# Performance work log

Measured on AMD Instinct MI355X. Metric: run time of the kernel, lower is better.

Reference implementation:

```python
import jax, jax.numpy as jnp
from jax import lax
import numpy as np

R = 4            # search_range
B, H, W, C = 8, 192, 192, 64
CV = (2 * R + 1) ** 2          # 81 cost-volume channels
CIN0 = CV + 2 * C              # concat(cost, prv, nxt) channels = 209
FILTERS = (128, 64, 32, 16)
DN = ('NHWC', 'HWIO', 'NHWC')
EPS = 1e-3                     # Keras BatchNormalization default epsilon


def setup_inputs() -> dict:
    key = jax.random.key(0)
    ks = iter(jax.random.split(key, 32))
    inp = {}
    inp['prv'] = jax.random.normal(next(ks), (B, H, W, C), jnp.float32)
    inp['nxt'] = jax.random.normal(next(ks), (B, H, W, C), jnp.float32)
    cin = CIN0
    for i, f in enumerate(FILTERS):
        inp[f'dw{i}'] = jax.random.normal(next(ks), (3, 3, 1, cin), jnp.float32) / np.sqrt(9.0)
        inp[f'pw{i}'] = jax.random.normal(next(ks), (1, 1, cin, f), jnp.float32) / np.sqrt(cin)
        inp[f'b{i}'] = jnp.zeros((f,), jnp.float32)
        cin = f
    inp['bn_gamma'] = jnp.ones((cin,), jnp.float32)
    inp['bn_beta'] = jnp.zeros((cin,), jnp.float32)
    inp['bn_mean'] = jnp.zeros((cin,), jnp.float32)
    inp['bn_var'] = jnp.ones((cin,), jnp.float32)
    inp['flow_w'] = jax.random.normal(next(ks), (3, 3, cin, 2), jnp.float32) / np.sqrt(9.0 * cin)
    return inp


def mish(x):
    return x * jnp.tanh(jax.nn.softplus(x))


def cost_volume(prv, nxt):
    # pad nxt by R on spatial dims, correlate over (2R+1)^2 shifts
    pad = jnp.pad(nxt, ((0, 0), (R, R), (R, R), (0, 0)))
    vols = []
    for i in range(2 * R + 1):           # fixed 9x9 offset set (not a data dim)
        for j in range(2 * R + 1):
            roi = lax.slice(pad, (0, i, j, 0), (B, i + H, j + W, C))
            vols.append(jnp.mean(prv * roi, axis=-1))
    cv = jnp.stack(vols, axis=-1)        # [B,H,W,81]
    return jax.nn.leaky_relu(cv, 0.1)


def sep_conv(x, dw, pw, b):
    cin = x.shape[-1]
    y = lax.conv_general_dilated(x, dw, (1, 1), 'SAME',
                                 dimension_numbers=DN, feature_group_count=cin)
    y = lax.conv_general_dilated(y, pw, (1, 1), 'SAME', dimension_numbers=DN) + b
    return mish(y)


def reference(prv, nxt, dw0, pw0, b0, dw1, pw1, b1, dw2, pw2, b2, dw3, pw3, b3,
              bn_gamma, bn_beta, bn_mean, bn_var, flow_w):
    cost = cost_volume(prv, nxt)
    x = jnp.concatenate([cost, prv, nxt], axis=-1)   # [B,H,W,209]
    for dw, pw, b in ((dw0, pw0, b0), (dw1, pw1, b1), (dw2, pw2, b2), (dw3, pw3, b3)):
        x = sep_conv(x, dw, pw, b)
    # BatchNorm (inference: moving statistics)
    x = (x - bn_mean) * (bn_gamma / jnp.sqrt(bn_var + EPS)) + bn_beta
    flow = lax.conv_general_dilated(x, flow_w, (1, 1), 'SAME', dimension_numbers=DN)
    scale = (float(H) ** 2 + float(W) ** 2) ** 0.5
    return scale * flow
```

## Files before the change

kernel.cpp:

```cpp
#include <hip/hip_runtime.h>
#include <hip/hip_bf16.h>

#define BB 8
#define HH 192
#define WW 192
#define CC0 64
#define NPIX (BB*HH*WW)
#define NCV 81
#define CVP 96

typedef __attribute__((ext_vector_type(8))) short short8;
typedef __attribute__((ext_vector_type(4))) short short4v;
typedef __attribute__((ext_vector_type(4))) float f32x4;

__device__ __forceinline__ float bf2f(short s) {
    union { unsigned u; float f; } x; x.u = ((unsigned)(unsigned short)s) << 16; return x.f;
}
__device__ __forceinline__ short f2bf(float f) {
    __hip_bfloat16 h = __float2bfloat16(f);
    return *reinterpret_cast<short*>(&h);
}
__device__ __forceinline__ void cvt8(const short8 iv, float* fv) {
    const int* ip = (const int*)&iv;
#pragma unroll
    for (int e = 0; e < 4; ++e) {
        union { unsigned u; float f; } lo, hi;
        lo.u = ((unsigned)ip[e]) << 16;
        hi.u = ((unsigned)ip[e]) & 0xffff0000u;
        fv[2 * e] = lo.f; fv[2 * e + 1] = hi.f;
    }
}

__device__ __forceinline__ float mish_f(float v) {
    if (v > 20.0f) return v;
    const float u = __expf(v);
    const float n = u * (u + 2.0f);
    return v * n / (n + 2.0f);
}

__global__ __launch_bounds__(256) void prep_kernel(
    const float* __restrict__ dw0, const float* __restrict__ pw0,
    const float* __restrict__ dw1, const float* __restrict__ pw1,
    const float* __restrict__ dw2, const float* __restrict__ pw2,
    const float* __restrict__ dw3, const float* __restrict__ pw3,
    __hip_bfloat16* __restrict__ wout)
{
    const int u = blockIdx.x * 256 + threadIdx.x;
    if (u >= 43456) return;
    float v = 0.f;
    if (u < 2016) {
        const int t = u / 224, c = u % 224;
        if (c < 64)       v = dw0[t*209 + 81  + c];
        else if (c < 128) v = dw0[t*209 + 145 + (c-64)];
        else if (c < 209) v = dw0[t*209 + (c-128)];
    } else if (u < 3168) {
        const int r = u-2016, t = r/128, c = r%128; v = dw1[t*128+c];
    } else if (u < 3744) {
        const int r = u-3168, t = r/64, c = r%64; v = dw2[t*64+c];
    } else if (u < 4032) {
        const int r = u-3744, t = r/32, c = r%32; v = dw3[t*32+c];
    } else if (u < 32704) {
        const int r = u-4032, n = r/224, c = r%224;
        if (c < 64)       v = pw0[(81+c)*128 + n];
        else if (c < 128) v = pw0[(145+(c-64))*128 + n];
        else if (c < 209) v = pw0[(c-128)*128 + n];
    } else if (u < 40896) {
        const int r = u-32704, n = r/128, c = r%128; v = pw1[c*64 + n];
    } else if (u < 42944) {
        const int r = u-40896, n = r/64, c = r%64; v = pw2[c*32 + n];
    } else {
        const int r = u-42944, n = r/32, c = r%32; v = pw3[c*16 + n];
    }
    wout[u] = __float2bfloat16(v);
}

__global__ __launch_bounds__(256) void prep2_kernel(
    const float* __restrict__ dw0, const float* __restrict__ dw1,
    const float* __restrict__ dw2, const float* __restrict__ dw3,
    const float* __restrict__ bn_g, const float* __restrict__ bn_b,
    const float* __restrict__ bn_m, const float* __restrict__ bn_v,
    const float* __restrict__ fw, float* __restrict__ fout)
{
    const int u = blockIdx.x * 256 + threadIdx.x;
    if (u >= 4338) return;
    float v = 0.f;
    if (u < 2016) {
        const int t = u / 224, c = u % 224;
        if (c < 64)       v = dw0[t*209 + 81  + c];
        else if (c < 128) v = dw0[t*209 + 145 + (c-64)];
        else if (c < 209) v = dw0[t*209 + (c-128)];
    } else if (u < 3168) {
        const int r = u-2016, t = r/128, c = r%128; v = dw1[t*128+c];
    } else if (u < 3744) {
        const int r = u-3168, t = r/64, c = r%64; v = dw2[t*64+c];
    } else if (u < 4032) {
        const int r = u-3744, t = r/32, c = r%32; v = dw3[t*32+c];
    } else if (u < 4320) {
        const int r = u-4032, t = r/32, rem = r%32, c = rem >> 1, s = rem & 1;
        const float sc = bn_g[c] * rsqrtf(bn_v[c] + 1e-3f);
        v = sc * fw[t*32 + c*2 + s];
    } else {
        const int r = u-4320, t = r/2, s = r%2;
        float a = 0.f;
        for (int c = 0; c < 16; ++c) {
            const float sc = bn_g[c] * rsqrtf(bn_v[c] + 1e-3f);
            const float sh = bn_b[c] - bn_m[c] * sc;
            a += sh * fw[t*32 + c*2 + s];
        }
        v = a;
    }
    fout[u] = v;
}

template<int UNIFIED>
__global__ __launch_bounds__(256) void cost_mfma_kernel(
    const float* __restrict__ prv, const float* __restrict__ nxt,
    __hip_bfloat16* __restrict__ xout)
{
    constexpr int OST   = UNIFIED ? 224 : CVP;
    constexpr int CVOFF = UNIFIED ? 128 : 0;

    __shared__ __align__(16) short sNxt[2][48][70];
    __shared__ __align__(16) short sCv[4][32][96];

    const int tid  = threadIdx.x;
    const int lane = tid & 63;
    const int wv   = tid >> 6;
    const int ln15 = lane & 15;
    const int kq   = lane >> 4;
    const int mt   = wv & 1;
    const int jt   = wv >> 1;

    const int bx = blockIdx.x;
    const int tw = bx % 6;
    const int th = (bx / 6) % 48;
    const int b  = bx / 288;
    const int w0 = tw * 32, h0 = th * 4;

    {
        const short8 z = {0,0,0,0,0,0,0,0};
#pragma unroll
        for (int t = 0; t < 6; ++t) {
            const int idx = tid + t * 256;
            const int row = idx / 384, rem = idx % 384;
            const int px = rem / 12, c8 = rem % 12;
            *(short8*)&sCv[row][px][c8 * 8] = z;
        }
    }

    short8 af0[4], af1[4];
    {
        const int apx = w0 + mt * 16 + ln15;
#pragma unroll
        for (int r4 = 0; r4 < 4; ++r4) {
            const float* ap = prv + (((size_t)b * HH + h0 + r4) * WW + apx) * CC0 + kq * 8;
            const float4 x0 = *(const float4*)(ap);
            const float4 x1 = *(const float4*)(ap + 4);
            const float4 x2 = *(const float4*)(ap + 32);
            const float4 x3 = *(const float4*)(ap + 36);
            af0[r4][0]=f2bf(x0.x); af0[r4][1]=f2bf(x0.y); af0[r4][2]=f2bf(x0.z); af0[r4][3]=f2bf(x0.w);
            af0[r4][4]=f2bf(x1.x); af0[r4][5]=f2bf(x1.y); af0[r4][6]=f2bf(x1.z); af0[r4][7]=f2bf(x1.w);
            af1[r4][0]=f2bf(x2.x); af1[r4][1]=f2bf(x2.y); af1[r4][2]=f2bf(x2.z); af1[r4][3]=f2bf(x2.w);
            af1[r4][4]=f2bf(x3.x); af1[r4][5]=f2bf(x3.y); af1[r4][6]=f2bf(x3.z); af1[r4][7]=f2bf(x3.w);
        }
    }

    const int s_px = (tid & 0xFF) >> 4;

    int cur = 0;
    {
        const int y0 = h0 - 4;
        if ((unsigned)y0 < (unsigned)HH) {
            const float* rowp = nxt + (((size_t)b * HH + y0) * WW) * CC0;
#pragma unroll
            for (int t = 0; t < 3; ++t) {
                const int u = tid + t * 256;
                if (u < 640) {
                    const int px = u >> 4, c4 = u & 15;
                    const int gw = w0 - 4 + px;
                    float4 v = make_float4(0.f, 0.f, 0.f, 0.f);
                    if ((unsigned)gw < (unsigned)WW)
                        v = *(const float4*)(rowp + (size_t)gw * CC0 + c4 * 4);
                    short4v sv;
                    sv[0]=f2bf(v.x); sv[1]=f2bf(v.y); sv[2]=f2bf(v.z); sv[3]=f2bf(v.w);
                    *(short4v*)&sNxt[0][px][c4 * 4] = sv;
                }
            }
        }
    }

    const size_t obase_blk = (((size_t)b * HH + h0) * WW + w0);

    for (int i = 0; i < 12; ++i) {
        const int y = h0 - 4 + i;
        const bool yok = ((unsigned)y < (unsigned)HH);
        __syncthreads();

        const int yn = y + 1;
        const bool nok = (i < 11) && ((unsigned)yn < (unsigned)HH);
        float4 sreg[3];
        if (nok) {
            const float* rowp = nxt + (((size_t)b * HH + yn) * WW) * CC0;
#pragma unroll
            for (int t = 0; t < 3; ++t) {
                const int u = tid + t * 256;
                sreg[t] = make_float4(0.f, 0.f, 0.f, 0.f);
                if (u < 640) {
                    const int px = u >> 4, c4 = u & 15;
                    const int gw = w0 - 4 + px;
                    if ((unsigned)gw < (unsigned)WW)
                        sreg[t] = *(const float4*)(rowp + (size_t)gw * CC0 + c4 * 4);
                }
            }
        }

        if (yok) {
            const int nb = mt * 16 + jt * 16 + ln15;
            const short* bp = &sNxt[cur][nb][kq * 8];
            const short8 b0 = *(const short8*)bp;
            const short8 b1 = *(const short8*)(bp + 32);
#pragma unroll
            for (int r4 = 0; r4 < 4; ++r4) {
                const int h = h0 + r4;
                const int rband = y - h + 4;
                if ((unsigned)rband <= 8u) {
                    f32x4 acc = {0.f, 0.f, 0.f, 0.f};
                    acc = __builtin_amdgcn_mfma_f32_16x16x32_bf16(af0[r4], b0, acc, 0, 0, 0);
                    acc = __builtin_amdgcn_mfma_f32_16x16x32_bf16(af1[r4], b1, acc, 0, 0, 0);
#pragma unroll
                    for (int rr = 0; rr < 4; ++rr) {
                        const int m_local = kq * 4 + rr;
                        const int dj = jt * 16 + ln15 - m_local;
                        if ((unsigned)dj < 9u) {
                            float mv = acc[rr] * (1.0f / 64.0f);
                            mv = (mv > 0.f) ? mv : 0.1f * mv;
                            sCv[r4][mt * 16 + m_local][rband * 9 + dj] = f2bf(mv);
                        }
                    }
                }
            }
            if (UNIFIED && y >= h0 && y < h0 + 4) {
                const int px_o = tid >> 3, cg = tid & 7;
                short* op = (short*)xout + (((size_t)b * HH + y) * WW + w0 + px_o) * OST
                            + 64 + cg * 8;
                *(short8*)op = *(const short8*)&sNxt[cur][4 + px_o][cg * 8];
            }
        }

        if (nok) {
#pragma unroll
            for (int t = 0; t < 3; ++t) {
                const int u = tid + t * 256;
                if (u < 640) {
                    const int px = u >> 4, c4 = u & 15;
                    short4v sv;
                    sv[0]=f2bf(sreg[t].x); sv[1]=f2bf(sreg[t].y);
                    sv[2]=f2bf(sreg[t].z); sv[3]=f2bf(sreg[t].w);
                    *(short4v*)&sNxt[cur ^ 1][px][c4 * 4] = sv;
                }
            }
        }
        cur ^= 1;
    }

    __syncthreads();
#pragma unroll
    for (int t = 0; t < 6; ++t) {
        const int idx = tid + t * 256;
        const int row = idx / 384, rem = idx % 384;
        const int px = rem / 12, c8 = rem % 12;
        short* op = (short*)xout + (obase_blk + (size_t)row * WW + px) * OST + CVOFF + c8 * 8;
        *(short8*)op = *(const short8*)&sCv[row][px][c8 * 8];
    }
    if (UNIFIED) {
#pragma unroll
        for (int t = 0; t < 4; ++t) {
            const int u = tid + t * 256;
            const int row = u >> 8, px = (u >> 3) & 31, cg = u & 7;
            const float* ap = prv + (obase_blk + (size_t)row * WW + px) * CC0 + cg * 8;
            const float4 x0 = *(const float4*)(ap);
            const float4 x1 = *(const float4*)(ap + 4);
            short8 v;
            v[0]=f2bf(x0.x); v[1]=f2bf(x0.y); v[2]=f2bf(x0.z); v[3]=f2bf(x0.w);
            v[4]=f2bf(x1.x); v[5]=f2bf(x1.y); v[6]=f2bf(x1.z); v[7]=f2bf(x1.w);
            short* op = (short*)xout + (obase_blk + (size_t)row * WW + px) * OST + cg * 8;
            *(short8*)op = v;
        }
    }
}

template<int KP, int COUT, int MODE>
__global__ __launch_bounds__(256) void sepconv_mfma(
    const __hip_bfloat16* __restrict__ in,
    const float* __restrict__ prv, const float* __restrict__ nxt,
    const float* __restrict__ dwf,
    const __hip_bfloat16* __restrict__ Bt,
    const float* __restrict__ bias,
    __hip_bfloat16* __restrict__ out)
{
    constexpr int NT  = COUT / 16;
    constexpr int WGN = (NT >= 2) ? 2 : 1;
    constexpr int WGM = 4 / WGN;
    constexpr int TM  = 8 / WGM;
    constexpr int TN  = NT / WGN;

    __shared__ __align__(16) short sIn[6][34][32];
    __shared__ __align__(16) short sA[4][128][8];
    __shared__ __align__(16) short sB[4][COUT][8];

    const int tid  = threadIdx.x;
    const int lane = tid & 63;
    const int wv   = tid >> 6;
    const int ln15 = lane & 15;
    const int kq   = lane >> 4;
    const int wm   = wv % WGM;
    const int wn   = wv / WGM;

    const int bx = blockIdx.x;
    const int tw = bx % 6;
    const int th = (bx / 6) % 48;
    const int bb = bx / 288;
    const int w0 = tw * 32, h0 = th * 4;

    const int dkbu = __builtin_amdgcn_readfirstlane(wv);
    const int dww  = lane & 31;
    const int dhh  = (lane >> 5) * 2;

    f32x4 acc[TM][TN] = {};

    for (int k0 = 0; k0 < KP; k0 += 32) {
        for (int u = tid; u < 816; u += 256) {
            const int kb = u & 3;
            const int p  = u >> 2;
            const int iw = p % 34, ih = p / 34;
            const int gw = w0 - 1 + iw, gh = h0 - 1 + ih;
            short8 v = {0,0,0,0,0,0,0,0};
            if ((unsigned)gw < (unsigned)WW && (unsigned)gh < (unsigned)HH) {
                const size_t pix = ((size_t)bb * HH + gh) * WW + gw;
                const int c0 = k0 + kb * 8;
                if (MODE == 0) {
                    v = *(const short8*)((const short*)in + pix * KP + c0);
                } else {
                    if (c0 < 64) {
                        const float4* s = (const float4*)(prv + pix * 64 + c0);
                        const float4 a = s[0], bq = s[1];
                        v[0]=f2bf(a.x);  v[1]=f2bf(a.y);  v[2]=f2bf(a.z);  v[3]=f2bf(a.w);
                        v[4]=f2bf(bq.x); v[5]=f2bf(bq.y); v[6]=f2bf(bq.z); v[7]=f2bf(bq.w);
                    } else if (c0 < 128) {
                        const float4* s = (const float4*)(nxt + pix * 64 + (c0 - 64));
                        const float4 a = s[0], bq = s[1];
                        v[0]=f2bf(a.x);  v[1]=f2bf(a.y);  v[2]=f2bf(a.z);  v[3]=f2bf(a.w);
                        v[4]=f2bf(bq.x); v[5]=f2bf(bq.y); v[6]=f2bf(bq.z); v[7]=f2bf(bq.w);
                    } else {
                        v = *(const short8*)((const short*)in + pix * CVP + (c0 - 128));
                    }
                }
            }
            *(short8*)&sIn[ih][iw][kb * 8] = v;
        }
        for (int u = tid; u < COUT * 4; u += 256) {
            const int n = u >> 2, kb = u & 3;
            short8 v = *(const short8*)((const short*)Bt + (size_t)n * KP + k0 + kb * 8);
            *(short8*)&sB[kb][n ^ (kb << 2)][0] = v;
        }
        __syncthreads();

        {
            const float* wrow = dwf + k0 + dkbu * 8;
            float r0[8] = {0,0,0,0,0,0,0,0};
            float r1[8] = {0,0,0,0,0,0,0,0};
#pragma unroll
            for (int dy = 0; dy < 4; ++dy) {
#pragma unroll
                for (int dx = 0; dx < 3; ++dx) {
                    const short8 iv = *(const short8*)&sIn[dhh + dy][dww + dx][dkbu * 8];
                    float fv[8];
                    cvt8(iv, fv);
                    if (dy < 3) {
#pragma unroll
                        for (int j = 0; j < 8; ++j)
                            r0[j] += fv[j] * wrow[(dy * 3 + dx) * KP + j];
                    }
                    if (dy >= 1) {
#pragma unroll
                        for (int j = 0; j < 8; ++j)
                            r1[j] += fv[j] * wrow[((dy - 1) * 3 + dx) * KP + j];
                    }
                }
            }
            const int px0 = dhh * 32 + dww;
            short8 o0, o1;
#pragma unroll
            for (int j = 0; j < 8; ++j) { o0[j] = f2bf(r0[j]); o1[j] = f2bf(r1[j]); }
            *(short8*)&sA[dkbu][px0 ^ (dkbu << 2)][0] = o0;
            *(short8*)&sA[dkbu][(px0 + 32) ^ (dkbu << 2)][0] = o1;
        }
        __syncthreads();

        short8 af[TM], bf8[TN];
#pragma unroll
        for (int i = 0; i < TM; ++i) {
            const int m = (wm * TM + i) * 16 + ln15;
            af[i] = *(const short8*)&sA[kq][m ^ (kq << 2)][0];
        }
#pragma unroll
        for (int j = 0; j < TN; ++j) {
            const int n = (wn * TN + j) * 16 + ln15;
            bf8[j] = *(const short8*)&sB[kq][n ^ (kq << 2)][0];
        }
#pragma unroll
        for (int i = 0; i < TM; ++i)
#pragma unroll
            for (int j = 0; j < TN; ++j)
                acc[i][j] = __builtin_amdgcn_mfma_f32_16x16x32_bf16(
                    af[i], bf8[j], acc[i][j], 0, 0, 0);
        __syncthreads();
    }

#pragma unroll
    for (int j = 0; j < TN; ++j) {
        const int n = (wn * TN + j) * 16 + ln15;
        const float bj = bias[n];
#pragma unroll
        for (int i = 0; i < TM; ++i) {
#pragma unroll
            for (int r = 0; r < 4; ++r) {
                const int m  = (wm * TM + i) * 16 + kq * 4 + r;
                const int gh = h0 + (m >> 5), gw = w0 + (m & 31);
                const size_t gp = ((size_t)bb * HH + gh) * WW + gw;
                out[gp * COUT + n] = __float2bfloat16(mish_f(acc[i][j][r] + bj));
            }
        }
    }
}

__global__ __launch_bounds__(256) void bn_flow_kernel(
    const __hip_bfloat16* __restrict__ xin,
    const float* __restrict__ fwp, const float* __restrict__ tbv,
    float* __restrict__ out)
{
    const int pix = blockIdx.x * 256 + threadIdx.x;
    const int wq  = pix % WW;
    const int hq  = (pix / WW) % HH;
    const int bq  = pix / (WW * HH);
    float a0 = 0.f, a1 = 0.f;
#pragma unroll
    for (int dy = -1; dy <= 1; ++dy) {
        const int yy = hq + dy;
        if ((unsigned)yy >= HH) continue;
#pragma unroll
        for (int dx = -1; dx <= 1; ++dx) {
            const int xx = wq + dx;
            if ((unsigned)xx >= WW) continue;
            const int t = (dy + 1) * 3 + (dx + 1);
            a0 += tbv[t * 2 + 0];
            a1 += tbv[t * 2 + 1];
            const short* xp = (const short*)xin + (((size_t)bq * HH + yy) * WW + xx) * 16;
            const short8 v0 = *(const short8*)xp;
            const short8 v1 = *(const short8*)(xp + 8);
            float x[16];
            cvt8(v0, x); cvt8(v1, x + 8);
            const float* wp = fwp + t * 32;
#pragma unroll
            for (int c = 0; c < 16; ++c) {
                a0 += x[c] * wp[c * 2 + 0];
                a1 += x[c] * wp[c * 2 + 1];
            }
        }
    }
    const float SC = sqrtf((float)(HH * HH + WW * WW));
    out[(size_t)pix * 2 + 0] = SC * a0;
    out[(size_t)pix * 2 + 1] = SC * a1;
}

extern "C" void kernel_launch(void* const* d_in, const int* in_sizes, int n_in,
                              void* d_out, int out_size, void* d_ws, size_t ws_size,
                              hipStream_t stream)
{
    const float* prv   = (const float*)d_in[0];
    const float* nxt   = (const float*)d_in[1];
    const float* dw0   = (const float*)d_in[2];
    const float* pw0   = (const float*)d_in[3];
    const float* b0    = (const float*)d_in[4];
    const float* dw1   = (const float*)d_in[5];
    const float* pw1   = (const float*)d_in[6];
    const float* b1    = (const float*)d_in[7];
    const float* dw2   = (const float*)d_in[8];
    const float* pw2   = (const float*)d_in[9];
    const float* b2    = (const float*)d_in[10];
    const float* dw3   = (const float*)d_in[11];
    const float* pw3   = (const float*)d_in[12];
    const float* b3    = (const float*)d_in[13];
    const float* bn_g  = (const float*)d_in[14];
    const float* bn_b  = (const float*)d_in[15];
    const float* bn_m  = (const float*)d_in[16];
    const float* bn_v  = (const float*)d_in[17];
    const float* fw    = (const float*)d_in[18];
    float* outp = (float*)d_out;

    const size_t N = (size_t)NPIX;
    __hip_bfloat16* ws = (__hip_bfloat16*)d_ws;

    const size_t need_uni = (N * 352 + 43456) * 2 + 4338 * 4;
    const bool uni = (ws_size >= need_uni);

    __hip_bfloat16* t1  = uni ? (ws + N * 224) : (ws + N * 96);
    __hip_bfloat16* wts = uni ? (ws + N * 352) : (ws + N * 224);
    __hip_bfloat16* t2  = ws;
    __hip_bfloat16* t3  = t1;
    __hip_bfloat16* t4  = ws + N * 64;
    __hip_bfloat16* Bt0 = wts + 4032;
    __hip_bfloat16* Bt1 = wts + 32704;
    __hip_bfloat16* Bt2 = wts + 40896;
    __hip_bfloat16* Bt3 = wts + 42944;
    float* fwt = (float*)(wts + 43456);

    prep_kernel<<<170, 256, 0, stream>>>(dw0, pw0, dw1, pw1, dw2, pw2, dw3, pw3, wts);
    prep2_kernel<<<17, 256, 0, stream>>>(dw0, dw1, dw2, dw3,
                                         bn_g, bn_b, bn_m, bn_v, fw, fwt);
    if (uni) {
        cost_mfma_kernel<1><<<2304, 256, 0, stream>>>(prv, nxt, ws);
        sepconv_mfma<224, 128, 0><<<2304, 256, 0, stream>>>(ws, nullptr, nullptr,
                                                            fwt, Bt0, b0, t1);
    } else {
        cost_mfma_kernel<0><<<2304, 256, 0, stream>>>(prv, nxt, ws);
        sepconv_mfma<224, 128, 1><<<2304, 256, 0, stream>>>(ws, prv, nxt,
                                                            fwt, Bt0, b0, t1);
    }
    sepconv_mfma<128, 64, 0><<<2304, 256, 0, stream>>>(t1, nullptr, nullptr,
                                                       fwt + 2016, Bt1, b1, t2);
    sepconv_mfma<64, 32, 0><<<2304, 256, 0, stream>>>(t2, nullptr, nullptr,
                                                      fwt + 3168, Bt2, b2, t3);
    sepconv_mfma<32, 16, 0><<<2304, 256, 0, stream>>>(t3, nullptr, nullptr,
                                                      fwt + 3744, Bt3, b3, t4);
    bn_flow_kernel<<<NPIX / 256, 256, 0, stream>>>(t4, fwt + 4032, fwt + 4320, outp);
}
```

Measured before the change: 537.5 us.

## Prefetch next input chunk into registers and read pointwise weights directly

In the separable-conv MFMA kernel, the K loop is fully unrolled and the haloed input tile for the next 32-channel chunk is loaded into registers while the current chunk is processed. This overlaps global loads with the depthwise and MFMA work. The pointwise weight fragments are now loaded straight from global memory into registers, which removes the sB shared buffer and its staging. The trailing barrier is also dropped, since the next iteration's barrier already orders the shared-memory reuse. The cost is higher register pressure and scattered global weight reads instead of shared-memory reads.

```diff
diff --git a/kernel.cpp b/kernel.cpp
--- a/kernel.cpp
+++ b/kernel.cpp
@@ -165,8 +165,6 @@
         }
     }
 
-    const int s_px = (tid & 0xFF) >> 4;
-
     int cur = 0;
     {
         const int y0 = h0 - 4;
@@ -298,6 +296,7 @@
     const float* __restrict__ bias,
     __hip_bfloat16* __restrict__ out)
 {
+    constexpr int NC  = KP / 32;
     constexpr int NT  = COUT / 16;
     constexpr int WGN = (NT >= 2) ? 2 : 1;
     constexpr int WGM = 4 / WGN;
@@ -306,7 +305,6 @@
 
     __shared__ __align__(16) short sIn[6][34][32];
     __shared__ __align__(16) short sA[4][128][8];
-    __shared__ __align__(16) short sB[4][COUT][8];
 
     const int tid  = threadIdx.x;
     const int lane = tid & 63;
@@ -326,44 +324,68 @@
     const int dww  = lane & 31;
     const int dhh  = (lane >> 5) * 2;
 
+    auto load_unit = [&](int u, int k0) -> short8 {
+        const int kb = u & 3;
+        const int p  = u >> 2;
+        const int iw = p % 34, ih = p / 34;
+        const int gw = w0 - 1 + iw, gh = h0 - 1 + ih;
+        short8 v = {0,0,0,0,0,0,0,0};
+        if ((unsigned)gw < (unsigned)WW && (unsigned)gh < (unsigned)HH) {
+            const size_t pix = ((size_t)bb * HH + gh) * WW + gw;
+            const int c0 = k0 + kb * 8;
+            if (MODE == 0) {
+                v = *(const short8*)((const short*)in + pix * KP + c0);
+            } else {
+                if (c0 < 64) {
+                    const float4* s = (const float4*)(prv + pix * 64 + c0);
+                    const float4 a = s[0], bq = s[1];
+                    v[0]=f2bf(a.x);  v[1]=f2bf(a.y);  v[2]=f2bf(a.z);  v[3]=f2bf(a.w);
+                    v[4]=f2bf(bq.x); v[5]=f2bf(bq.y); v[6]=f2bf(bq.z); v[7]=f2bf(bq.w);
+                } else if (c0 < 128) {
+                    const float4* s = (const float4*)(nxt + pix * 64 + (c0 - 64));
+                    const float4 a = s[0], bq = s[1];
+                    v[0]=f2bf(a.x);  v[1]=f2bf(a.y);  v[2]=f2bf(a.z);  v[3]=f2bf(a.w);
+                    v[4]=f2bf(bq.x); v[5]=f2bf(bq.y); v[6]=f2bf(bq.z); v[7]=f2bf(bq.w);
+                } else {
+                    v = *(const short8*)((const short*)in + pix * CVP + (c0 - 128));
+                }
+            }
+        }
+        return v;
+    };
+
     f32x4 acc[TM][TN] = {};
-
-    for (int k0 = 0; k0 < KP; k0 += 32) {
-        for (int u = tid; u < 816; u += 256) {
-            const int kb = u & 3;
-            const int p  = u >> 2;
-            const int iw = p % 34, ih = p / 34;
-            const int gw = w0 - 1 + iw, gh = h0 - 1 + ih;
-            short8 v = {0,0,0,0,0,0,0,0};
-            if ((unsigned)gw < (unsigned)WW && (unsigned)gh < (unsigned)HH) {
-                const size_t pix = ((size_t)bb * HH + gh) * WW + gw;
-                const int c0 = k0 + kb * 8;
-                if (MODE == 0) {
-                    v = *(const short8*)((const short*)in + pix * KP + c0);
-                } else {
-                    if (c0 < 64) {
-                        const float4* s = (const float4*)(prv + pix * 64 + c0);
-                        const float4 a = s[0], bq = s[1];
-                        v[0]=f2bf(a.x);  v[1]=f2bf(a.y);  v[2]=f2bf(a.z);  v[3]=f2bf(a.w);
-                        v[4]=f2bf(bq.x); v[5]=f2bf(bq.y); v[6]=f2bf(bq.z); v[7]=f2bf(bq.w);
-                    } else if (c0 < 128) {
-                        const float4* s = (const float4*)(nxt + pix * 64 + (c0 - 64));
-                        const float4 a = s[0], bq = s[1];
-                        v[0]=f2bf(a.x);  v[1]=f2bf(a.y);  v[2]=f2bf(a.z);  v[3]=f2bf(a.w);
-                        v[4]=f2bf(bq.x); v[5]=f2bf(bq.y); v[6]=f2bf(bq.z); v[7]=f2bf(bq.w);
-                    } else {
-                        v = *(const short8*)((const short*)in + pix * CVP + (c0 - 128));
-                    }
-                }
-            }
-            *(short8*)&sIn[ih][iw][kb * 8] = v;
-        }
-        for (int u = tid; u < COUT * 4; u += 256) {
-            const int n = u >> 2, kb = u & 3;
-            short8 v = *(const short8*)((const short*)Bt + (size_t)n * KP + k0 + kb * 8);
-            *(short8*)&sB[kb][n ^ (kb << 2)][0] = v;
+    short8 pr[4];
+
+#pragma unroll
+    for (int t = 0; t < 4; ++t) {
+        const int u = tid + t * 256;
+        pr[t] = (u < 816) ? load_unit(u, 0) : short8{0,0,0,0,0,0,0,0};
+    }
+
+#pragma unroll
+    for (int c = 0; c < NC; ++c) {
+        const int k0 = c * 32;
+#pragma unroll
+        for (int t = 0; t < 4; ++t) {
+            const int u = tid + t * 256;
+            if (u < 816) *(short8*)((short*)sIn + (size_t)u * 8) = pr[t];
         }
         __syncthreads();
+
+        if (c + 1 < NC) {
+#pragma unroll
+            for (int t = 0; t < 4; ++t) {
+                const int u = tid + t * 256;
+                if (u < 816) pr[t] = load_unit(u, k0 + 32);
+            }
+        }
+        short8 bfr[TN];
+#pragma unroll
+        for (int j = 0; j < TN; ++j) {
+            const int n = (wn * TN + j) * 16 + ln15;
+            bfr[j] = *(const short8*)((const short*)Bt + (size_t)n * KP + k0 + kq * 8);
+        }
 
         {
             const float* wrow = dwf + k0 + dkbu * 8;
@@ -397,24 +419,18 @@
         }
         __syncthreads();
 
-        short8 af[TM], bf8[TN];
+        short8 af[TM];
 #pragma unroll
         for (int i = 0; i < TM; ++i) {
             const int m = (wm * TM + i) * 16 + ln15;
             af[i] = *(const short8*)&sA[kq][m ^ (kq << 2)][0];
         }
 #pragma unroll
-        for (int j = 0; j < TN; ++j) {
-            const int n = (wn * TN + j) * 16 + ln15;
-            bf8[j] = *(const short8*)&sB[kq][n ^ (kq << 2)][0];
-        }
-#pragma unroll
         for (int i = 0; i < TM; ++i)
 #pragma unroll
             for (int j = 0; j < TN; ++j)
                 acc[i][j] = __builtin_amdgcn_mfma_f32_16x16x32_bf16(
-                    af[i], bf8[j], acc[i][j], 0, 0, 0);
-        __syncthreads();
+                    af[i], bfr[j], acc[i][j], 0, 0, 0);
     }
 
 #pragma unroll
```

Result: faster. 488.1 us (-9.2%).
